# Kernel tuning notes

Hardware: AMD Instinct MI355X
Metric: run time of the kernel (lower is better)

Reference implementation:

```python
import jax, jax.numpy as jnp
import numpy as np
import math

DIM = 768
NUM_HEADS = 16
PERHEAD = DIM // NUM_HEADS  # 48
B, T = 4, 2048


def setup_inputs() -> dict:
    key = jax.random.key(0)
    k_x, k_wi, k_bi, k_wo, k_bo = jax.random.split(key, 5)
    s_in = 1.0 / math.sqrt(DIM)
    return {
        "x": jax.random.normal(k_x, (B, T, DIM), dtype=jnp.float32),
        # linear_in: y = x @ w_in + b_in, w_in: (DIM, 3*DIM)
        "w_in": jax.random.uniform(k_wi, (DIM, 3 * DIM), jnp.float32, -s_in, s_in),
        "b_in": jax.random.uniform(k_bi, (3 * DIM,), jnp.float32, -s_in, s_in),
        "w_out": jax.random.uniform(k_wo, (DIM, DIM), jnp.float32, -s_in, s_in),
        "b_out": jax.random.uniform(k_bo, (DIM,), jnp.float32, -s_in, s_in),
    }


def reference(x, w_in, b_in, w_out, b_out):
    bs, tok, _ = x.shape
    qkv = x @ w_in + b_in                                   # (B, T, 3*DIM)
    # Faithful to torch: reshape to (B, T, H, 3*ph), move heads, chunk last dim.
    qkv = qkv.reshape(bs, tok, NUM_HEADS, 3 * PERHEAD)
    qkv = jnp.transpose(qkv, (0, 2, 1, 3))                  # (B, H, T, 3*ph)
    q, k, v = jnp.split(qkv, 3, axis=-1)                    # each (B, H, T, ph)
    scale = 1.0 / math.sqrt(PERHEAD)
    scores = jnp.einsum("bhqd,bhkd->bhqk", q, k) * scale    # (B, H, T, T)
    attn = jax.nn.softmax(scores, axis=-1)
    # dropout p=0.0 (eval) -> identity
    out = jnp.einsum("bhqk,bhkd->bhqd", attn, v)            # (B, H, T, ph)
    out = jnp.transpose(out, (0, 2, 1, 3)).reshape(bs, tok, DIM)
    return out @ w_out + b_out
```

## Files before the change

kernel.cpp:

```cpp
#include <hip/hip_runtime.h>
#include <hip/hip_bf16.h>
#include <math.h>

typedef __attribute__((ext_vector_type(8))) short short8;
typedef __attribute__((ext_vector_type(4))) float floatx4;
typedef __hip_bfloat16 bf16;

#define DIM 768
#define NHEADS 16
#define PH 48
#define VROWS 49
#define BATCH 4
#define SEQ 2048
#define MTOK (BATCH*SEQ)
#define NQKV (3*DIM)
#define NQK (2*DIM)
#define LOG2E 1.44269504088896f
#define CFAC (0.14433756729740643f * LOG2E)

#define NB_CAST   6144
#define NB_TWIN   1728
#define NB_TWOUT  576
#define NB_MISC   140

__device__ __forceinline__ void cp16(void* dst, const void* src) {
    *(float4*)dst = *(const float4*)src;
}
__device__ __forceinline__ unsigned short f2us(float v) {
    bf16 b = __float2bfloat16(v);
    return *(unsigned short*)&b;
}
__device__ __forceinline__ float us2f(unsigned short u) {
    bf16 b = *(bf16*)&u;
    return __bfloat162float(b);
}
__device__ __forceinline__ void gload_lds16(const bf16* g, bf16* l) {
    __builtin_amdgcn_global_load_lds(
        (const __attribute__((address_space(1))) unsigned int*)g,
        (__attribute__((address_space(3))) unsigned int*)l, 16, 0, 0);
}

__global__ void sniff_dtype(const unsigned short* __restrict__ x, int* flag) {
    float v = us2f(x[threadIdx.x]);
    int bad = !(fabsf(v) < 64.0f);
    int any_bad = __any(bad);
    if (threadIdx.x == 0) *flag = any_bad ? 1 : 0;
}

__global__ __launch_bounds__(256) void prep_all(
    const void* __restrict__ x, const void* __restrict__ w_in,
    const void* __restrict__ w_out, const void* __restrict__ bin,
    const void* __restrict__ bout,
    bf16* __restrict__ xb, bf16* __restrict__ winT, bf16* __restrict__ woutT,
    float* __restrict__ bi, float* __restrict__ bo, bf16* __restrict__ Vt,
    const int* __restrict__ flag)
{
    __shared__ bf16 tile[32][33];
    const int bid = blockIdx.x, tid = threadIdx.x;
    const bool f32 = (*flag != 0);

    if (bid < NB_CAST) {
        int i = bid * 256 + tid;
        if (f32) {
            float4 v = ((const float4*)x)[i];
            ushort4 o;
            o.x = f2us(v.x); o.y = f2us(v.y); o.z = f2us(v.z); o.w = f2us(v.w);
            ((ushort4*)xb)[i] = o;
        } else {
            ((ushort4*)xb)[i] = ((const ushort4*)x)[i];
        }
    } else if (bid < NB_CAST + NB_TWIN + NB_TWOUT) {
        const void* in; bf16* out; int R, C, tt;
        if (bid < NB_CAST + NB_TWIN) {
            in = w_in; out = winT; R = DIM; C = NQKV; tt = bid - NB_CAST;
        } else {
            in = w_out; out = woutT; R = DIM; C = DIM; tt = bid - NB_CAST - NB_TWIN;
        }
        int ctiles = C / 32;
        int c0 = (tt % ctiles) * 32, r0 = (tt / ctiles) * 32;
        int tx = tid & 31, ty = tid >> 5;
#pragma unroll
        for (int j = 0; j < 4; j++) {
            size_t idx = (size_t)(r0 + ty + 8*j) * C + c0 + tx;
            float v = f32 ? ((const float*)in)[idx]
                          : us2f(((const unsigned short*)in)[idx]);
            tile[ty + 8*j][tx] = __float2bfloat16(v);
        }
        __syncthreads();
#pragma unroll
        for (int j = 0; j < 4; j++)
            out[(size_t)(c0 + ty + 8*j) * R + r0 + tx] = tile[tx][ty + 8*j];
    } else {
        int t = (bid - (NB_CAST + NB_TWIN + NB_TWOUT)) * 256 + tid;
        if (t < NQKV) {
            bi[t] = f32 ? ((const float*)bin)[t] : us2f(((const unsigned short*)bin)[t]);
        } else if (t < NQKV + DIM) {
            int j = t - NQKV;
            bo[j] = f32 ? ((const float*)bout)[j] : us2f(((const unsigned short*)bout)[j]);
        } else {
            int k = t - (NQKV + DIM);
            int bh = k >> 9, pos = (k & 511) * 4;
            bf16* dst = Vt + ((size_t)bh * VROWS + 48) * SEQ + pos;
            ushort4 ones;
            ones.x = ones.y = ones.z = ones.w = f2us(1.0f);
            *(ushort4*)dst = ones;
        }
    }
}

template<int N, int MODE>
__global__ __launch_bounds__(256) void gemm_bias(
    const bf16* __restrict__ A, const bf16* __restrict__ BT,
    const float* __restrict__ bias, void* __restrict__ C0, bf16* __restrict__ Vc,
    const int* __restrict__ flag)
{
    constexpr int K = 768;
    __shared__ __align__(16) bf16 As[128 * 32];
    __shared__ __align__(16) bf16 Bs[128 * 32];
    const bool out_f32 = (MODE == 2) && (*flag != 0);
    const int tid = threadIdx.x;
    const int id = blockIdx.x;
    const int m0 = (id & 63) * 128, n0 = (id >> 6) * 128;
    const int w = tid >> 6, lane = tid & 63, lq = lane >> 4, ln = lane & 15;
    const int wr = w & 1, wc = w >> 1;

    const int rl0 = w * 32 + (lane >> 2);
    const int rl1 = rl0 + 16;
    const int ssw = ((lane >> 2) ^ (lane >> 4)) & 3;
    const int cm = (lane & 3) ^ ssw;
    const bf16* gA0 = A + (size_t)(m0 + rl0) * K + cm * 8;
    const bf16* gA1 = A + (size_t)(m0 + rl1) * K + cm * 8;
    const bf16* gB0 = BT + (size_t)(n0 + rl0) * K + cm * 8;
    const bf16* gB1 = BT + (size_t)(n0 + rl1) * K + cm * 8;
    bf16* lA0 = &As[(w * 32 + 0) * 32];
    bf16* lA1 = &As[(w * 32 + 16) * 32];
    bf16* lB0 = &Bs[(w * 32 + 0) * 32];
    bf16* lB1 = &Bs[(w * 32 + 16) * 32];

    const int rsw = (ln ^ (ln >> 2)) & 3;
    const int rchunk = (lq ^ rsw) * 8;

    floatx4 zero4 = {0.f, 0.f, 0.f, 0.f};
    floatx4 acc[4][4];
#pragma unroll
    for (int mi = 0; mi < 4; mi++)
#pragma unroll
        for (int nj = 0; nj < 4; nj++) acc[mi][nj] = zero4;

    for (int k0 = 0; k0 < K; k0 += 32) {
        gload_lds16(gA0, lA0);
        gload_lds16(gA1, lA1);
        gload_lds16(gB0, lB0);
        gload_lds16(gB1, lB1);
        gA0 += 32; gA1 += 32; gB0 += 32; gB1 += 32;
        __syncthreads();

        short8 a[4], b[4];
#pragma unroll
        for (int mi = 0; mi < 4; mi++)
            a[mi] = *(const short8*)&As[(wr * 64 + 16 * mi + ln) * 32 + rchunk];
#pragma unroll
        for (int nj = 0; nj < 4; nj++)
            b[nj] = *(const short8*)&Bs[(wc * 64 + 16 * nj + ln) * 32 + rchunk];
#pragma unroll
        for (int mi = 0; mi < 4; mi++)
#pragma unroll
            for (int nj = 0; nj < 4; nj++)
                acc[mi][nj] = __builtin_amdgcn_mfma_f32_16x16x32_bf16(
                    a[mi], b[nj], acc[mi][nj], 0, 0, 0);
        __syncthreads();
    }

#pragma unroll
    for (int nj = 0; nj < 4; nj++) {
        int n = n0 + wc * 64 + 16 * nj + ln;
        float bv = bias[n];
        if (MODE == 2) {
#pragma unroll
            for (int mi = 0; mi < 4; mi++)
#pragma unroll
                for (int i = 0; i < 4; i++) {
                    size_t off = (size_t)(m0 + wr * 64 + 16 * mi + 4 * lq + i) * N + n;
                    float val = acc[mi][nj][i] + bv;
                    if (out_f32) ((float*)C0)[off] = val;
                    else         ((bf16*)C0)[off] = __float2bfloat16(val);
                }
        } else {
            int h = n / 144, r = n - 144 * h;
            if (r < 96) {
                float sc = (r < 48) ? CFAC : 1.0f;
#pragma unroll
                for (int mi = 0; mi < 4; mi++)
#pragma unroll
                    for (int i = 0; i < 4; i++) {
                        size_t off = (size_t)(m0 + wr * 64 + 16 * mi + 4 * lq + i) * NQK
                                     + h * 96 + r;
                        ((bf16*)C0)[off] = __float2bfloat16((acc[mi][nj][i] + bv) * sc);
                    }
            } else {
                int d = r - 96;
#pragma unroll
                for (int mi = 0; mi < 4; mi++)
#pragma unroll
                    for (int i = 0; i < 4; i++) {
                        size_t off = (size_t)(m0 + wr * 64 + 16 * mi + 4 * lq + i) * DIM
                                     + h * PH + d;
                        Vc[off] = __float2bfloat16(acc[mi][nj][i] + bv);
                    }
            }
        }
    }
}

__global__ __launch_bounds__(256) void v_transpose(
    const bf16* __restrict__ Vc, bf16* __restrict__ Vt)
{
    __shared__ unsigned short tile[48][72];
    const int id = blockIdx.x, tid = threadIdx.x;
    const int g = id & 63, t0 = (id >> 6) * 64;
    const int h = g & 15, b = g >> 4;

#pragma unroll
    for (int s = 0; s < 3; s++) {
        int idx = tid + 256 * s;
        int r = idx / 12, q4 = (idx % 12) * 4;
        ushort4 v = *(const ushort4*)&Vc[((size_t)(b * SEQ + t0 + r)) * DIM + h * PH + q4];
        tile[q4 + 0][r] = v.x;
        tile[q4 + 1][r] = v.y;
        tile[q4 + 2][r] = v.z;
        tile[q4 + 3][r] = v.w;
    }
    __syncthreads();

#pragma unroll
    for (int s = 0; s < 3; s++) {
        int idx = tid + 256 * s;
        int d = idx >> 4, jc = (idx & 15) * 4;
        ushort4 o;
        o.x = tile[d][16 * ((jc + 0) & 3) + ((jc + 0) >> 2)];
        o.y = tile[d][16 * ((jc + 1) & 3) + ((jc + 1) >> 2)];
        o.z = tile[d][16 * ((jc + 2) & 3) + ((jc + 2) >> 2)];
        o.w = tile[d][16 * ((jc + 3) & 3) + ((jc + 3) >> 2)];
        *(ushort4*)&Vt[((size_t)(b * NHEADS + h) * VROWS + d) * SEQ + t0 + jc] = o;
    }
}

__global__ __launch_bounds__(256, 4) void attn_fused(
    const bf16* __restrict__ QK, const bf16* __restrict__ Vt, bf16* __restrict__ O)
{
    __shared__ bf16 QPs[128][72];
    __shared__ bf16 Ks[64][72];
    __shared__ bf16 VsT[64][72];

    const int tid = threadIdx.x;
    const int id = blockIdx.x;
    const int g = id & 63, qt = id >> 6;
    const int h = g & 15, b = g >> 4;
    const int w = tid >> 6, lane = tid & 63, lq = lane >> 4, ln = lane & 15;
    const size_t rowbase = (size_t)b * SEQ;
    const int q0 = qt * 128;
    const int hoff = h * 96;
    const bf16* Vth = Vt + (size_t)(b * NHEADS + h) * VROWS * SEQ;

    const bf16 bzero = __float2bfloat16(0.f);
    for (int idx = tid; idx < 2048; idx += 256)
        QPs[idx >> 4][48 + (idx & 15)] = bzero;
    for (int idx = tid; idx < 1024; idx += 256)
        Ks[idx >> 4][48 + (idx & 15)] = bzero;

#pragma unroll
    for (int s = 0; s < 3; s++) {
        int idx = tid + 256 * s, r = idx / 6, c = idx % 6;
        cp16(&QPs[r][c * 8], &QK[(rowbase + q0 + r) * NQK + hoff + c * 8]);
    }
    __syncthreads();

    short8 qa0A = *(const short8*)&QPs[16*w + ln][lq * 8];
    short8 qa1A = *(const short8*)&QPs[16*w + ln][lq * 8 + 32];
    short8 qa0B = *(const short8*)&QPs[64 + 16*w + ln][lq * 8];
    short8 qa1B = *(const short8*)&QPs[64 + 16*w + ln][lq * 8 + 32];

    const int kr0a = tid / 6, kc0a = tid % 6;
    const int kr1a = (tid + 256) / 6, kc1a = (tid + 256) % 6;
    const char* kg0 = (const char*)(QK + (rowbase + kr0a) * NQK + hoff + 48) + kc0a * 16;
    const char* kg1 = (const char*)(QK + (rowbase + kr1a) * NQK + hoff + 48) + kc1a * 16;
    bf16* kd0 = &Ks[kr0a][kc0a * 8];
    bf16* kd1 = &Ks[kr1a][kc1a * 8];
    const bool kact = (tid < 128);
    const int vr0 = tid >> 3, vc0 = tid & 7;
    const char* vg0 = (const char*)(Vth + (size_t)vr0 * SEQ) + vc0 * 16;
    const char* vg1 = (const char*)(Vth + (size_t)(32 + vr0) * SEQ) + vc0 * 16;
    bf16* vd0 = &VsT[vr0][vc0 * 8];
    bf16* vd1 = &VsT[32 + vr0][vc0 * 8];
    const bool vact = (tid < 136);
    const ptrdiff_t KADV = (ptrdiff_t)64 * NQK * 2;
    const ptrdiff_t VADV = 128;

    floatx4 zero4 = {0.f, 0.f, 0.f, 0.f};
    floatx4 oA[4], oB[4];
#pragma unroll
    for (int nt = 0; nt < 4; nt++) { oA[nt] = zero4; oB[nt] = zero4; }

    float4 rk0, rk1, rv0, rv1;
    rk0 = *(const float4*)kg0;
    if (kact) rk1 = *(const float4*)kg1;
    rv0 = *(const float4*)vg0;
    if (vact) rv1 = *(const float4*)vg1;
    kg0 += KADV; kg1 += KADV; vg0 += VADV; vg1 += VADV;

    for (int kt = 0; kt < 32; kt++) {
        __syncthreads();
        *(float4*)kd0 = rk0;
        if (kact) *(float4*)kd1 = rk1;
        *(float4*)vd0 = rv0;
        if (vact) *(float4*)vd1 = rv1;
        if (kt < 31) {
            rk0 = *(const float4*)kg0;
            if (kact) rk1 = *(const float4*)kg1;
            rv0 = *(const float4*)vg0;
            if (vact) rv1 = *(const float4*)vg1;
            kg0 += KADV; kg1 += KADV; vg0 += VADV; vg1 += VADV;
        }
        __syncthreads();

        floatx4 sA[4], sB[4];
#pragma unroll
        for (int t = 0; t < 4; t++) { sA[t] = zero4; sB[t] = zero4; }
#pragma unroll
        for (int t = 0; t < 4; t++) {
            short8 b0 = *(const short8*)&Ks[16*t + ln][lq * 8];
            short8 b1 = *(const short8*)&Ks[16*t + ln][lq * 8 + 32];
            sA[t] = __builtin_amdgcn_mfma_f32_16x16x32_bf16(qa0A, b0, sA[t], 0, 0, 0);
            sA[t] = __builtin_amdgcn_mfma_f32_16x16x32_bf16(qa1A, b1, sA[t], 0, 0, 0);
            sB[t] = __builtin_amdgcn_mfma_f32_16x16x32_bf16(qa0B, b0, sB[t], 0, 0, 0);
            sB[t] = __builtin_amdgcn_mfma_f32_16x16x32_bf16(qa1B, b1, sB[t], 0, 0, 0);
        }

#pragma unroll
        for (int i = 0; i < 4; i++) {
            union { ushort4 u4; __hip_bfloat162 h2[2]; } pk;
            float2 p01, p23;
            p01.x = __builtin_amdgcn_exp2f(sA[0][i]);
            p01.y = __builtin_amdgcn_exp2f(sA[1][i]);
            p23.x = __builtin_amdgcn_exp2f(sA[2][i]);
            p23.y = __builtin_amdgcn_exp2f(sA[3][i]);
            pk.h2[0] = __float22bfloat162_rn(p01);
            pk.h2[1] = __float22bfloat162_rn(p23);
            *(ushort4*)&QPs[16*w + 4*lq + i][4*ln] = pk.u4;
        }
#pragma unroll
        for (int i = 0; i < 4; i++) {
            union { ushort4 u4; __hip_bfloat162 h2[2]; } pk;
            float2 p01, p23;
            p01.x = __builtin_amdgcn_exp2f(sB[0][i]);
            p01.y = __builtin_amdgcn_exp2f(sB[1][i]);
            p23.x = __builtin_amdgcn_exp2f(sB[2][i]);
            p23.y = __builtin_amdgcn_exp2f(sB[3][i]);
            pk.h2[0] = __float22bfloat162_rn(p01);
            pk.h2[1] = __float22bfloat162_rn(p23);
            *(ushort4*)&QPs[64 + 16*w + 4*lq + i][4*ln] = pk.u4;
        }

#pragma unroll
        for (int ks = 0; ks < 2; ks++) {
            short8 paA = *(const short8*)&QPs[16*w + ln][lq * 8 + 32*ks];
            short8 paB = *(const short8*)&QPs[64 + 16*w + ln][lq * 8 + 32*ks];
#pragma unroll
            for (int nt = 0; nt < 4; nt++) {
                short8 vb = *(const short8*)&VsT[16*nt + ln][lq * 8 + 32*ks];
                oA[nt] = __builtin_amdgcn_mfma_f32_16x16x32_bf16(paA, vb, oA[nt], 0, 0, 0);
                oB[nt] = __builtin_amdgcn_mfma_f32_16x16x32_bf16(paB, vb, oB[nt], 0, 0, 0);
            }
        }
    }

#pragma unroll
    for (int i = 0; i < 4; i++) {
        float lA = __shfl(oA[3][i], (lane >> 4) << 4);
        float lB = __shfl(oB[3][i], (lane >> 4) << 4);
        float invA = 1.0f / lA, invB = 1.0f / lB;
        int rowA = q0 + 16*w + 4*lq + i;
        int rowB = rowA + 64;
#pragma unroll
        for (int nt = 0; nt < 3; nt++) {
            O[(rowbase + rowA) * DIM + h * PH + 16*nt + ln] =
                __float2bfloat16(oA[nt][i] * invA);
            O[(rowbase + rowB) * DIM + h * PH + 16*nt + ln] =
                __float2bfloat16(oB[nt][i] * invB);
        }
    }
}

extern "C" void kernel_launch(void* const* d_in, const int* in_sizes, int n_in,
                              void* d_out, int out_size, void* d_ws, size_t ws_size,
                              hipStream_t stream) {
    const void* x     = d_in[0];
    const void* w_in  = d_in[1];
    const void* b_in  = d_in[2];
    const void* w_out = d_in[3];
    const void* b_out = d_in[4];

    bf16* qk    = (bf16*)d_ws;
    bf16* Vt    = qk    + (size_t)MTOK * NQK;
    bf16* xb    = Vt    + (size_t)BATCH * NHEADS * VROWS * SEQ;
    bf16* attn  = xb;
    bf16* winT  = xb    + (size_t)MTOK * DIM;
    bf16* woutT = winT  + (size_t)NQKV * DIM;
    bf16* Vc    = woutT + (size_t)DIM * DIM;
    float* bi   = (float*)(Vc + (size_t)MTOK * DIM);
    float* bo   = bi + NQKV;
    int* flag   = (int*)(bo + DIM);

    sniff_dtype<<<1, 64, 0, stream>>>((const unsigned short*)x, flag);
    prep_all<<<NB_CAST + NB_TWIN + NB_TWOUT + NB_MISC, 256, 0, stream>>>(
        x, w_in, w_out, b_in, b_out, xb, winT, woutT, bi, bo, Vt, flag);

    gemm_bias<NQKV, 1><<<64 * (NQKV/128), 256, 0, stream>>>(xb, winT, bi, qk, Vc, flag);
    v_transpose<<<64 * (SEQ/64), 256, 0, stream>>>(Vc, Vt);
    attn_fused<<<64 * (SEQ/128), 256, 0, stream>>>(qk, Vt, attn);
    gemm_bias<DIM, 2><<<64 * (DIM/128), 256, 0, stream>>>(attn, woutT, bo, d_out, nullptr, flag);
}
```

Before: 243.6 us.

## Fuse V transpose into QKV GEMM epilogue and inline dtype sniffing

The QKV projection GEMM now stages its V columns in shared memory, reusing the A/B tile buffers after the K loop. It then writes them directly into the head-major transposed Vt layout, with the same intra-64-token permutation that attention expects. This removes the separate v_transpose kernel and the round trip of the intermediate Vc buffer through global memory. The standalone dtype-sniff kernel is also dropped: each kernel that needs to know the input dtype re-checks the first 64 input values with a wave vote. The cost is an extra LDS pass and barrier in the GEMM epilogue, plus redundant sniff loads in every block.

```diff
diff --git a/kernel.cpp b/kernel.cpp
--- a/kernel.cpp
+++ b/kernel.cpp
@@ -39,12 +39,10 @@
         (const __attribute__((address_space(1))) unsigned int*)g,
         (__attribute__((address_space(3))) unsigned int*)l, 16, 0, 0);
 }
-
-__global__ void sniff_dtype(const unsigned short* __restrict__ x, int* flag) {
-    float v = us2f(x[threadIdx.x]);
+__device__ __forceinline__ bool sniff_f32(const unsigned short* __restrict__ x) {
+    float v = us2f(x[threadIdx.x & 63]);
     int bad = !(fabsf(v) < 64.0f);
-    int any_bad = __any(bad);
-    if (threadIdx.x == 0) *flag = any_bad ? 1 : 0;
+    return __any(bad) != 0;
 }
 
 __global__ __launch_bounds__(256) void prep_all(
@@ -52,12 +50,11 @@
     const void* __restrict__ w_out, const void* __restrict__ bin,
     const void* __restrict__ bout,
     bf16* __restrict__ xb, bf16* __restrict__ winT, bf16* __restrict__ woutT,
-    float* __restrict__ bi, float* __restrict__ bo, bf16* __restrict__ Vt,
-    const int* __restrict__ flag)
+    float* __restrict__ bi, float* __restrict__ bo, bf16* __restrict__ Vt)
 {
     __shared__ bf16 tile[32][33];
     const int bid = blockIdx.x, tid = threadIdx.x;
-    const bool f32 = (*flag != 0);
+    const bool f32 = sniff_f32((const unsigned short*)x);
 
     if (bid < NB_CAST) {
         int i = bid * 256 + tid;
@@ -111,13 +108,14 @@
 template<int N, int MODE>
 __global__ __launch_bounds__(256) void gemm_bias(
     const bf16* __restrict__ A, const bf16* __restrict__ BT,
-    const float* __restrict__ bias, void* __restrict__ C0, bf16* __restrict__ Vc,
-    const int* __restrict__ flag)
+    const float* __restrict__ bias, void* __restrict__ C0, bf16* __restrict__ Vt,
+    const unsigned short* __restrict__ xraw)
 {
     constexpr int K = 768;
-    __shared__ __align__(16) bf16 As[128 * 32];
-    __shared__ __align__(16) bf16 Bs[128 * 32];
-    const bool out_f32 = (MODE == 2) && (*flag != 0);
+    __shared__ __align__(16) bf16 smem[2 * 128 * 32];
+    bf16* As = smem;
+    bf16* Bs = smem + 128 * 32;
+    const bool out_f32 = (MODE == 2) && sniff_f32(xraw);
     const int tid = threadIdx.x;
     const int id = blockIdx.x;
     const int m0 = (id & 63) * 128, n0 = (id >> 6) * 128;
@@ -170,6 +168,7 @@
                     a[mi], b[nj], acc[mi][nj], 0, 0, 0);
         __syncthreads();
     }
+    bf16 (*VLs)[136] = (bf16(*)[136])smem;
 
 #pragma unroll
     for (int nj = 0; nj < 4; nj++) {
@@ -202,46 +201,28 @@
 #pragma unroll
                 for (int mi = 0; mi < 4; mi++)
 #pragma unroll
-                    for (int i = 0; i < 4; i++) {
-                        size_t off = (size_t)(m0 + wr * 64 + 16 * mi + 4 * lq + i) * DIM
-                                     + h * PH + d;
-                        Vc[off] = __float2bfloat16(acc[mi][nj][i] + bv);
-                    }
+                    for (int i = 0; i < 4; i++)
+                        VLs[d][wr * 64 + 16 * lq + 4 * i + mi] =
+                            __float2bfloat16(acc[mi][nj][i] + bv);
             }
         }
     }
-}
-
-__global__ __launch_bounds__(256) void v_transpose(
-    const bf16* __restrict__ Vc, bf16* __restrict__ Vt)
-{
-    __shared__ unsigned short tile[48][72];
-    const int id = blockIdx.x, tid = threadIdx.x;
-    const int g = id & 63, t0 = (id >> 6) * 64;
-    const int h = g & 15, b = g >> 4;
-
-#pragma unroll
-    for (int s = 0; s < 3; s++) {
-        int idx = tid + 256 * s;
-        int r = idx / 12, q4 = (idx % 12) * 4;
-        ushort4 v = *(const ushort4*)&Vc[((size_t)(b * SEQ + t0 + r)) * DIM + h * PH + q4];
-        tile[q4 + 0][r] = v.x;
-        tile[q4 + 1][r] = v.y;
-        tile[q4 + 2][r] = v.z;
-        tile[q4 + 3][r] = v.w;
-    }
-    __syncthreads();
-
-#pragma unroll
-    for (int s = 0; s < 3; s++) {
-        int idx = tid + 256 * s;
-        int d = idx >> 4, jc = (idx & 15) * 4;
-        ushort4 o;
-        o.x = tile[d][16 * ((jc + 0) & 3) + ((jc + 0) >> 2)];
-        o.y = tile[d][16 * ((jc + 1) & 3) + ((jc + 1) >> 2)];
-        o.z = tile[d][16 * ((jc + 2) & 3) + ((jc + 2) >> 2)];
-        o.w = tile[d][16 * ((jc + 3) & 3) + ((jc + 3) >> 2)];
-        *(ushort4*)&Vt[((size_t)(b * NHEADS + h) * VROWS + d) * SEQ + t0 + jc] = o;
+
+    if (MODE == 1) {
+        __syncthreads();
+        const int bidx = m0 >> 11, tok0 = m0 & 2047;
+#pragma unroll
+        for (int s = 0; s < 3; s++) {
+            int idx = tid + 256 * s;
+            int d = idx >> 4, ch = idx & 15;
+            int h = (n0 + 31 - d) / 144;
+            int n = 144 * h + 96 + d;
+            if (n >= n0 && n < n0 + 128) {
+                bf16* dst = Vt + ((size_t)(bidx * NHEADS + h) * VROWS + d) * SEQ
+                            + tok0 + ch * 8;
+                *(float4*)dst = *(const float4*)&VLs[d][ch * 8];
+            }
+        }
     }
 }
 
@@ -406,17 +387,15 @@
     bf16* attn  = xb;
     bf16* winT  = xb    + (size_t)MTOK * DIM;
     bf16* woutT = winT  + (size_t)NQKV * DIM;
-    bf16* Vc    = woutT + (size_t)DIM * DIM;
-    float* bi   = (float*)(Vc + (size_t)MTOK * DIM);
+    float* bi   = (float*)(woutT + (size_t)DIM * DIM);
     float* bo   = bi + NQKV;
-    int* flag   = (int*)(bo + DIM);
-
-    sniff_dtype<<<1, 64, 0, stream>>>((const unsigned short*)x, flag);
+
     prep_all<<<NB_CAST + NB_TWIN + NB_TWOUT + NB_MISC, 256, 0, stream>>>(
-        x, w_in, w_out, b_in, b_out, xb, winT, woutT, bi, bo, Vt, flag);
-
-    gemm_bias<NQKV, 1><<<64 * (NQKV/128), 256, 0, stream>>>(xb, winT, bi, qk, Vc, flag);
-    v_transpose<<<64 * (SEQ/64), 256, 0, stream>>>(Vc, Vt);
+        x, w_in, w_out, b_in, b_out, xb, winT, woutT, bi, bo, Vt);
+
+    gemm_bias<NQKV, 1><<<64 * (NQKV/128), 256, 0, stream>>>(
+        xb, winT, bi, qk, Vt, (const unsigned short*)x);
     attn_fused<<<64 * (SEQ/128), 256, 0, stream>>>(qk, Vt, attn);
-    gemm_bias<DIM, 2><<<64 * (DIM/128), 256, 0, stream>>>(attn, woutT, bo, d_out, nullptr, flag);
-}
+    gemm_bias<DIM, 2><<<64 * (DIM/128), 256, 0, stream>>>(
+        attn, woutT, bo, d_out, nullptr, (const unsigned short*)x);
+}
```

After: 230.2 us. -5.5%, faster.
